# Kernel tuning notes

Hardware: AMD Instinct MI355X
Metric: run time of the kernel (lower is better)

Reference implementation:

```python
import jax, jax.numpy as jnp
import numpy as np

N_NODES = 100000
N_EDGES = 3200000
NUM_GRAPHS = 512


def _glorot(key, shape):
    fan_in, fan_out = shape[0], shape[1]
    lim = float(np.sqrt(6.0 / (fan_in + fan_out)))
    return jax.random.uniform(key, shape, jnp.float32, -lim, lim)


def setup_inputs() -> dict:
    key = jax.random.key(0)
    ks = jax.random.split(key, 12)
    x = jax.random.normal(ks[0], (N_NODES, 3), jnp.float32)
    edge_index = jax.random.randint(ks[1], (2, N_EDGES), 0, N_NODES, jnp.int64)
    batch = jnp.sort(jax.random.randint(ks[2], (N_NODES,), 0, NUM_GRAPHS, jnp.int64))
    return {
        'x': x,
        'edge_index': edge_index,
        'batch': batch,
        'W1': _glorot(ks[3], (3, 32)), 'b1': jnp.zeros((32,), jnp.float32),
        'W2': _glorot(ks[4], (32, 64)), 'b2': jnp.zeros((64,), jnp.float32),
        'W3': _glorot(ks[5], (64, 64)), 'b3': jnp.zeros((64,), jnp.float32),
        'lW1': _glorot(ks[6], (64, 32)), 'lb1': jnp.zeros((32,), jnp.float32),
        'lW2': _glorot(ks[7], (32, 5)), 'lb2': jnp.zeros((5,), jnp.float32),
    }


def gcn_conv(x, src, dst, W, b, n):
    # PyG GCNConv: add self-loops, symmetric deg^{-1/2} normalization,
    # linear transform then gather-scale-scatter aggregation.
    loop = jnp.arange(n, dtype=src.dtype)
    s = jnp.concatenate([src, loop])
    d = jnp.concatenate([dst, loop])
    deg = jax.ops.segment_sum(jnp.ones_like(d, dtype=x.dtype), d, num_segments=n)
    dinv = jnp.where(deg > 0, jax.lax.rsqrt(deg), 0.0)
    norm = dinv[s] * dinv[d]  # [E+N]
    h = x @ W                 # [N, out]
    out = jax.ops.segment_sum(h[s] * norm[:, None], d, num_segments=n)
    return out + b


def reference(x, edge_index, batch, W1, b1, W2, b2, W3, b3, lW1, lb1, lW2, lb2):
    src, dst = edge_index[0], edge_index[1]
    n = x.shape[0]
    h = jax.nn.relu(gcn_conv(x, src, dst, W1, b1, n))
    h = jax.nn.relu(gcn_conv(h, src, dst, W2, b2, n))
    h = gcn_conv(h, src, dst, W3, b3, n)
    pooled = jax.ops.segment_sum(h, batch, num_segments=NUM_GRAPHS)  # [G, 64]
    z = jax.nn.relu(pooled @ lW1 + lb1)
    z = z @ lW2 + lb2
    # original applies log_softmax over dim=0 (the graph axis)
    return jax.nn.log_softmax(z, axis=0)
```

## Files before the change

kernel.cpp:

```cpp
#include <hip/hip_runtime.h>
#include <hip/hip_fp16.h>

#define N_GRAPHS 512
#define NB 1563
#define KNODE 64
#define CAP 3072
#define EPW 8192
#define NWMAX 400


__global__ void k_part2(const int4* __restrict__ src4, const int4* __restrict__ dst4,
                        unsigned* __restrict__ ebuf2, unsigned* __restrict__ P, int E, int nw) {
    __shared__ int dstc[EPW];
    __shared__ unsigned hist[NB];
    __shared__ unsigned tsum[256];
    int w = blockIdx.x, t = threadIdx.x;
    int e0 = w * EPW;
    int cnt = E - e0 < EPW ? E - e0 : EPW;
    int cnt4 = cnt >> 2;
    for (int i = t; i < NB; i += 256) hist[i] = 0;
    __syncthreads();
    const int4* d4 = dst4 + (e0 >> 2);
    const int4* s4 = src4 + (e0 >> 2);
    for (int i = t; i < cnt4; i += 256) {
        int4 d = d4[i];
        dstc[4 * i + 0] = d.x; dstc[4 * i + 1] = d.y;
        dstc[4 * i + 2] = d.z; dstc[4 * i + 3] = d.w;
        atomicAdd(&hist[d.x >> 6], 1u);
        atomicAdd(&hist[d.y >> 6], 1u);
        atomicAdd(&hist[d.z >> 6], 1u);
        atomicAdd(&hist[d.w >> 6], 1u);
    }
    __syncthreads();
    const int PT7 = 7;
    unsigned loc[PT7];
    int base = t * PT7;
    unsigned s = 0;
#pragma unroll
    for (int k = 0; k < PT7; ++k) {
        int idx = base + k;
        unsigned v = (idx < NB) ? hist[idx] : 0u;
        loc[k] = s;
        s += v;
    }
    tsum[t] = s;
    __syncthreads();
    for (int off = 1; off < 256; off <<= 1) {
        unsigned u = (t >= off) ? tsum[t - off] : 0u;
        __syncthreads();
        tsum[t] += u;
        __syncthreads();
    }
    unsigned toff = tsum[t] - s;
#pragma unroll
    for (int k = 0; k < PT7; ++k) {
        int idx = base + k;
        if (idx < NB) {
            unsigned cb = ((k < PT7 - 1) ? loc[k + 1] : s) - loc[k];
            unsigned st = toff + loc[k];
            P[(size_t)w * NB + idx] = (st << 16) | cb;
        }
    }
    __syncthreads();
#pragma unroll
    for (int k = 0; k < PT7; ++k) {
        int idx = base + k;
        if (idx < NB) hist[idx] = toff + loc[k];
    }
    __syncthreads();
    for (int i = t; i < cnt4; i += 256) {
        int4 sv = s4[i];
#pragma unroll
        for (int q = 0; q < 4; ++q) {
            int d = dstc[4 * i + q];
            int svv = q == 0 ? sv.x : q == 1 ? sv.y : q == 2 ? sv.z : sv.w;
            int bkt = d >> 6;
            unsigned pos = atomicAdd(&hist[bkt], 1u);
            ebuf2[(size_t)e0 + pos] = (unsigned)svv | ((unsigned)(d & 63) << 20);
        }
    }
}


__global__ void kT(const unsigned* __restrict__ P, unsigned* __restrict__ PT, int nw) {
    __shared__ unsigned tile[32][33];
    int bw = blockIdx.x;
    int bb = blockIdx.y;
    int tx = threadIdx.x & 31, ty = threadIdx.x >> 5;
#pragma unroll
    for (int r = 0; r < 32; r += 8) {
        int w = bw * 32 + ty + r;
        int b = bb * 32 + tx;
        tile[ty + r][tx] = (w < nw && b < NB) ? P[(size_t)w * NB + b] : 0u;
    }
    __syncthreads();
#pragma unroll
    for (int r = 0; r < 32; r += 8) {
        int b = bb * 32 + ty + r;
        int w = bw * 32 + tx;
        if (b < NB && w < nw) PT[(size_t)b * nw + w] = tile[tx][ty + r];
    }
}


__global__ void k_csr2(const unsigned* __restrict__ ebuf2, const unsigned* __restrict__ PT,
                       unsigned* __restrict__ ebufF, int* __restrict__ gCnt,
                       int2* __restrict__ rows, float* __restrict__ dinv, int n, int nw) {
    __shared__ unsigned ec[CAP];
    __shared__ unsigned info[NWMAX];
    __shared__ unsigned coff[NWMAX];
    __shared__ unsigned tsum[256];
    __shared__ int bins[KNODE], pfx[KNODE];
    int b = blockIdx.x, t = threadIdx.x;
    for (int w = t; w < nw; w += 256) info[w] = PT[(size_t)b * nw + w];
    __syncthreads();
    unsigned l0, l1, s = 0;
    {
        int i0 = t * 2, i1 = t * 2 + 1;
        unsigned v0 = (i0 < nw) ? (info[i0] & 0xFFFFu) : 0u;
        unsigned v1 = (i1 < nw) ? (info[i1] & 0xFFFFu) : 0u;
        l0 = 0; l1 = v0; s = v0 + v1;
    }
    tsum[t] = s;
    __syncthreads();
    for (int off = 1; off < 256; off <<= 1) {
        unsigned u = (t >= off) ? tsum[t - off] : 0u;
        __syncthreads();
        tsum[t] += u;
        __syncthreads();
    }
    unsigned toff = tsum[t] - s;
    {
        int i0 = t * 2, i1 = t * 2 + 1;
        if (i0 < nw) coff[i0] = toff + l0;
        if (i1 < nw) coff[i1] = toff + l1;
    }
    __syncthreads();
    int total = (int)tsum[255];
    int cnt = total < CAP ? total : CAP;
    if (t == 0) gCnt[b] = cnt;
    for (int w = t; w < nw; w += 256) {
        unsigned inf = info[w];
        unsigned st = inf >> 16, c = inf & 0xFFFFu;
        unsigned d0 = coff[w];
        const unsigned* src = ebuf2 + (size_t)w * EPW + st;
        for (unsigned k = 0; k < c; ++k) {
            unsigned p = d0 + k;
            if (p < (unsigned)CAP) ec[p] = src[k];
        }
    }
    if (t < KNODE) bins[t] = 0;
    __syncthreads();
    for (int i = t; i < cnt; i += 256) atomicAdd(&bins[ec[i] >> 20], 1);
    __syncthreads();
    if (t == 0) {
        int a = 0;
        for (int i = 0; i < KNODE; ++i) { pfx[i] = a; a += bins[i]; }
    }
    __syncthreads();
    if (t < KNODE) {
        int node = b * KNODE + t;
        if (node < n) {
            rows[node] = make_int2(b * CAP + pfx[t], bins[t]);
            dinv[node] = rsqrtf((float)(bins[t] + 1));
        }
    }
    if (t < KNODE) bins[t] = pfx[t];
    __syncthreads();
    for (int i = t; i < cnt; i += 256) {
        unsigned p = ec[i];
        int pp = atomicAdd(&bins[p >> 20], 1);
        ebufF[(size_t)b * CAP + pp] = p & 0xFFFFFu;
    }
}


__global__ void k_pre1(const float* __restrict__ x, const float* __restrict__ dinv,
                       float4* __restrict__ ts0, int n) {
    int i = blockIdx.x * 256 + threadIdx.x;
    if (i >= n) return;
    float d = dinv[i];
    ts0[i] = make_float4(d * x[3 * i], d * x[3 * i + 1], d * x[3 * i + 2], 0.f);
}


__global__ void k_agg1(const float4* __restrict__ ts0, const unsigned* __restrict__ esrc,
                       const int2* __restrict__ rows, const float* __restrict__ dinv,
                       float4* __restrict__ o1, int n) {
    int node = blockIdx.x * 256 + threadIdx.x;
    if (node >= n) return;
    int2 rc = rows[node];
    int s0 = rc.x, deg = rc.y;
    float4 a = ts0[node];
    int e = 0;
    for (; e + 4 <= deg; e += 4) {
        unsigned i0 = esrc[s0 + e + 0];
        unsigned i1 = esrc[s0 + e + 1];
        unsigned i2 = esrc[s0 + e + 2];
        unsigned i3 = esrc[s0 + e + 3];
        float4 v0 = ts0[i0], v1 = ts0[i1], v2 = ts0[i2], v3 = ts0[i3];
        a.x += v0.x + v1.x + v2.x + v3.x;
        a.y += v0.y + v1.y + v2.y + v3.y;
        a.z += v0.z + v1.z + v2.z + v3.z;
    }
    for (; e < deg; ++e) {
        float4 v = ts0[esrc[s0 + e]];
        a.x += v.x; a.y += v.y; a.z += v.z;
    }
    float d = dinv[node];
    o1[node] = make_float4(d * a.x, d * a.y, d * a.z, 0.f);
}


__global__ void k_t1(const float4* __restrict__ o1, const float* __restrict__ W1,
                     const float* __restrict__ b1, const float* __restrict__ dinv,
                     uint4* __restrict__ ts1, int n) {
    __shared__ float sW[96];
    __shared__ float sb[32];
    int t = threadIdx.x;
    if (t < 96) sW[t] = W1[t];
    if (t < 32) sb[t] = b1[t];
    __syncthreads();
    int ln = t >> 2, c = t & 3;
    int node = blockIdx.x * 64 + ln;
    if (node >= n) return;
    float4 o = o1[node];
    float d = dinv[node];
    float r[8];
#pragma unroll
    for (int k = 0; k < 8; ++k) {
        int j = c * 8 + k;
        float h = o.x * sW[j] + o.y * sW[32 + j] + o.z * sW[64 + j] + sb[j];
        r[k] = fmaxf(h, 0.f) * d;
    }
    __half2 h0 = __floats2half2_rn(r[0], r[1]);
    __half2 h1 = __floats2half2_rn(r[2], r[3]);
    __half2 h2 = __floats2half2_rn(r[4], r[5]);
    __half2 h3 = __floats2half2_rn(r[6], r[7]);
    uint4 w;
    w.x = *(unsigned*)&h0; w.y = *(unsigned*)&h1;
    w.z = *(unsigned*)&h2; w.w = *(unsigned*)&h3;
    ts1[(size_t)node * 4 + c] = w;
}


template <int NSLICE>
__global__ void k_aggW(const uint4* __restrict__ ts, const unsigned* __restrict__ ebuf,
                       const int* __restrict__ gCnt, const int2* __restrict__ rows,
                       const float* __restrict__ dinv, uint4* __restrict__ out, int n) {
    __shared__ unsigned eidx[CAP];
    __shared__ int cursor;
    int i = blockIdx.x;
    int b, slice;
    if (NSLICE == 1) {
        b = i; slice = 0;
    } else {
        int xcd = i & 7;
        slice = xcd & 1;
        b = (i >> 3) * 4 + (xcd >> 1);
    }
    if (b >= NB) return;
    int t = threadIdx.x;
    int cnt = gCnt[b];
    if (cnt > CAP) cnt = CAP;
    int bBase = b * CAP;
    const uint4* ebuf4 = (const uint4*)(ebuf + bBase);
    int cnt4 = (cnt + 3) >> 2;
    for (int k = t; k < cnt4; k += 128) ((uint4*)eidx)[k] = ebuf4[k];
    if (t == 0) cursor = 0;
    __syncthreads();

    const uint4* tss = ts + (size_t)slice * n * 4;
    int lane = t & 3;
    for (;;) {
        int my;
        if (lane == 0) my = atomicAdd(&cursor, 1);
        my = __shfl(my, 0, 4);
        if (my >= KNODE) break;
        int node = b * KNODE + my;
        if (node >= n) continue;
        int2 rc = rows[node];
        int ls = rc.x - bBase;
        int deg = rc.y;
        float2 a0, a1, a2, a3;
        {
            uint4 sv = tss[(size_t)node * 4 + lane];
            a0 = __half22float2(*(__half2*)&sv.x);
            a1 = __half22float2(*(__half2*)&sv.y);
            a2 = __half22float2(*(__half2*)&sv.z);
            a3 = __half22float2(*(__half2*)&sv.w);
        }
        int e = 0;
        for (; e + 4 <= deg; e += 4) {
            unsigned s0 = eidx[ls + e + 0];
            unsigned s1 = eidx[ls + e + 1];
            unsigned s2 = eidx[ls + e + 2];
            unsigned s3 = eidx[ls + e + 3];
            uint4 v0 = tss[(size_t)s0 * 4 + lane];
            uint4 v1 = tss[(size_t)s1 * 4 + lane];
            uint4 v2 = tss[(size_t)s2 * 4 + lane];
            uint4 v3 = tss[(size_t)s3 * 4 + lane];
            float2 f;
            f = __half22float2(*(__half2*)&v0.x); a0.x += f.x; a0.y += f.y;
            f = __half22float2(*(__half2*)&v0.y); a1.x += f.x; a1.y += f.y;
            f = __half22float2(*(__half2*)&v0.z); a2.x += f.x; a2.y += f.y;
            f = __half22float2(*(__half2*)&v0.w); a3.x += f.x; a3.y += f.y;
            f = __half22float2(*(__half2*)&v1.x); a0.x += f.x; a0.y += f.y;
            f = __half22float2(*(__half2*)&v1.y); a1.x += f.x; a1.y += f.y;
            f = __half22float2(*(__half2*)&v1.z); a2.x += f.x; a2.y += f.y;
            f = __half22float2(*(__half2*)&v1.w); a3.x += f.x; a3.y += f.y;
            f = __half22float2(*(__half2*)&v2.x); a0.x += f.x; a0.y += f.y;
            f = __half22float2(*(__half2*)&v2.y); a1.x += f.x; a1.y += f.y;
            f = __half22float2(*(__half2*)&v2.z); a2.x += f.x; a2.y += f.y;
            f = __half22float2(*(__half2*)&v2.w); a3.x += f.x; a3.y += f.y;
            f = __half22float2(*(__half2*)&v3.x); a0.x += f.x; a0.y += f.y;
            f = __half22float2(*(__half2*)&v3.y); a1.x += f.x; a1.y += f.y;
            f = __half22float2(*(__half2*)&v3.z); a2.x += f.x; a2.y += f.y;
            f = __half22float2(*(__half2*)&v3.w); a3.x += f.x; a3.y += f.y;
        }
        for (; e < deg; ++e) {
            unsigned s = eidx[ls + e];
            uint4 v = tss[(size_t)s * 4 + lane];
            float2 f;
            f = __half22float2(*(__half2*)&v.x); a0.x += f.x; a0.y += f.y;
            f = __half22float2(*(__half2*)&v.y); a1.x += f.x; a1.y += f.y;
            f = __half22float2(*(__half2*)&v.z); a2.x += f.x; a2.y += f.y;
            f = __half22float2(*(__half2*)&v.w); a3.x += f.x; a3.y += f.y;
        }
        float dd = dinv[node];
        __half2 o0 = __floats2half2_rn(dd * a0.x, dd * a0.y);
        __half2 o1 = __floats2half2_rn(dd * a1.x, dd * a1.y);
        __half2 o2 = __floats2half2_rn(dd * a2.x, dd * a2.y);
        __half2 o3 = __floats2half2_rn(dd * a3.x, dd * a3.y);
        uint4 w;
        w.x = *(unsigned*)&o0; w.y = *(unsigned*)&o1;
        w.z = *(unsigned*)&o2; w.w = *(unsigned*)&o3;
        out[(size_t)node * (NSLICE * 4) + slice * 4 + lane] = w;
    }
}


__global__ void k_t2(const uint4* __restrict__ o2, const float* __restrict__ W2,
                     const float* __restrict__ b2, const float* __restrict__ dinv,
                     uint4* __restrict__ ts2, int n) {
    __shared__ uint4 sO[128];
    __shared__ float sW[32 * 64];
    __shared__ float sb[64];
    int t = threadIdx.x;
    for (int i = t; i < 32 * 64; i += 256) sW[i] = W2[i];
    if (t < 64) sb[t] = b2[t];
    int node0 = blockIdx.x * 32;
    if (t < 128) {
        int nd = node0 + (t >> 2);
        sO[t] = (nd < n) ? o2[(size_t)node0 * 4 + t] : make_uint4(0, 0, 0, 0);
    }
    __syncthreads();
    int ln = t >> 3, c = t & 7;
    int node = node0 + ln;
    if (node >= n) return;
    const __half2* sOh = (const __half2*)sO;
    float acc[8];
#pragma unroll
    for (int k = 0; k < 8; ++k) acc[k] = sb[c * 8 + k];
#pragma unroll
    for (int i2 = 0; i2 < 16; ++i2) {
        float2 av = __half22float2(sOh[ln * 16 + i2]);
        const float* w0 = &sW[(2 * i2) * 64 + c * 8];
        const float* w1 = &sW[(2 * i2 + 1) * 64 + c * 8];
#pragma unroll
        for (int k = 0; k < 8; ++k) acc[k] += av.x * w0[k] + av.y * w1[k];
    }
    float d = dinv[node];
    float r[8];
#pragma unroll
    for (int k = 0; k < 8; ++k) r[k] = fmaxf(acc[k], 0.f) * d;
    __half2 h0 = __floats2half2_rn(r[0], r[1]);
    __half2 h1 = __floats2half2_rn(r[2], r[3]);
    __half2 h2 = __floats2half2_rn(r[4], r[5]);
    __half2 h3 = __floats2half2_rn(r[6], r[7]);
    uint4 w;
    w.x = *(unsigned*)&h0; w.y = *(unsigned*)&h1;
    w.z = *(unsigned*)&h2; w.w = *(unsigned*)&h3;
    ts2[((size_t)(c >> 2) * n + node) * 4 + (c & 3)] = w;
}


__global__ void k_pool(const __half2* __restrict__ h, const int* __restrict__ batch,
                       float* __restrict__ pooled, float* __restrict__ cntf, int n) {
    const int NBK = 32;
    int lane = threadIdx.x & 31;
    int sub = threadIdx.x >> 5;
    int n0 = (blockIdx.x * 8 + sub) * NBK;
    if (n0 >= n) return;
    int nend = n0 + NBK < n ? n0 + NBK : n;
    float2 acc = make_float2(0.f, 0.f);
    float rc = 0.f;
    int gcur = batch[n0];
    for (int i = n0; i < nend; ++i) {
        int g = batch[i];
        if (g != gcur) {
            atomicAdd(&pooled[gcur * 64 + 2 * lane], acc.x);
            atomicAdd(&pooled[gcur * 64 + 2 * lane + 1], acc.y);
            if (lane == 0) atomicAdd(&cntf[gcur], rc);
            acc = make_float2(0.f, 0.f);
            rc = 0.f;
            gcur = g;
        }
        float2 v = __half22float2(h[(size_t)i * 32 + lane]);
        acc.x += v.x;
        acc.y += v.y;
        rc += 1.f;
    }
    atomicAdd(&pooled[gcur * 64 + 2 * lane], acc.x);
    atomicAdd(&pooled[gcur * 64 + 2 * lane + 1], acc.y);
    if (lane == 0) atomicAdd(&cntf[gcur], rc);
}


#define GPB 4
__global__ void k_z(const float* __restrict__ P, const float* __restrict__ cntf,
                    const float* __restrict__ W3, const float* __restrict__ b3,
                    const float* __restrict__ lW1, const float* __restrict__ lb1,
                    const float* __restrict__ lW2, const float* __restrict__ lb2,
                    float* __restrict__ z) {
    __shared__ float sW3[64 * 64];
    __shared__ float sW1[64 * 32];
    __shared__ float sW2[32 * 5];
    __shared__ float sb3[64], sb1[32], sb2[5];
    __shared__ float sP[GPB][64];
    __shared__ float sH[GPB][64];
    __shared__ float sT[GPB][32];
    int t = threadIdx.x;
    for (int i = t; i < 64 * 64; i += 256) sW3[i] = W3[i];
    for (int i = t; i < 64 * 32; i += 256) sW1[i] = lW1[i];
    for (int i = t; i < 32 * 5; i += 256) sW2[i] = lW2[i];
    if (t < 64) sb3[t] = b3[t];
    if (t < 32) sb1[t] = lb1[t];
    if (t < 5) sb2[t] = lb2[t];
    int g0 = blockIdx.x * GPB;
    for (int i = t; i < GPB * 64; i += 256) sP[i >> 6][i & 63] = P[(size_t)g0 * 64 + i];
    __syncthreads();
    int lg = t >> 6;
    int j = t & 63;
    int g = g0 + lg;
    float cg = cntf[g];
    float a = cg * sb3[j];
#pragma unroll 8
    for (int i = 0; i < 64; ++i) a += sP[lg][i] * sW3[i * 64 + j];
    sH[lg][j] = a;
    __syncthreads();
    if (j < 32) {
        float a2 = sb1[j];
#pragma unroll 8
        for (int i = 0; i < 64; ++i) a2 += sH[lg][i] * sW1[i * 32 + j];
        sT[lg][j] = fmaxf(a2, 0.f);
    }
    __syncthreads();
    if (j < 5) {
        float a3 = sb2[j];
#pragma unroll
        for (int i = 0; i < 32; ++i) a3 += sT[lg][i] * sW2[i * 5 + j];
        z[g * 5 + j] = a3;
    }
}


__global__ void k_lsm(const float* __restrict__ z, float* __restrict__ out) {
    __shared__ float red[512];
    int g = threadIdx.x;
#pragma unroll
    for (int c = 0; c < 5; ++c) {
        float v = z[g * 5 + c];
        red[g] = v;
        __syncthreads();
        for (int off = 256; off > 0; off >>= 1) {
            if (g < off) red[g] = fmaxf(red[g], red[g + off]);
            __syncthreads();
        }
        float m = red[0];
        __syncthreads();
        red[g] = expf(v - m);
        __syncthreads();
        for (int off = 256; off > 0; off >>= 1) {
            if (g < off) red[g] += red[g + off];
            __syncthreads();
        }
        float lse = m + logf(red[0]);
        __syncthreads();
        out[g * 5 + c] = v - lse;
    }
}


extern "C" void kernel_launch(void* const* d_in, const int* in_sizes, int n_in,
                              void* d_out, int out_size, void* d_ws, size_t ws_size,
                              hipStream_t stream) {
    const float* x   = (const float*)d_in[0];
    const int* ei    = (const int*)d_in[1];
    const int* batch = (const int*)d_in[2];
    const float* W1  = (const float*)d_in[3];
    const float* b1  = (const float*)d_in[4];
    const float* W2  = (const float*)d_in[5];
    const float* b2  = (const float*)d_in[6];
    const float* W3  = (const float*)d_in[7];
    const float* b3  = (const float*)d_in[8];
    const float* lW1 = (const float*)d_in[9];
    const float* lb1 = (const float*)d_in[10];
    const float* lW2 = (const float*)d_in[11];
    const float* lb2 = (const float*)d_in[12];

    const int N = in_sizes[0] / 3;
    const int E = in_sizes[1] / 2;
    const int* src = ei;
    const int* dst = ei + E;
    const int nw = (E + EPW - 1) / EPW;

    char* ws = (char*)d_ws;
    size_t off = 0;
    auto alloc = [&](size_t bytes) -> void* {
        void* p = ws + off;
        off = (off + bytes + 255) & ~(size_t)255;
        return p;
    };

    int*      gCnt    = (int*)alloc((size_t)NB * 4);
    float*    dinv    = (float*)alloc((size_t)N * 4);
    int2*     rows    = (int2*)alloc((size_t)N * 8);
    unsigned* ebuf2   = (unsigned*)alloc((size_t)nw * EPW * 4);
    unsigned* P       = (unsigned*)alloc((size_t)nw * NB * 4);
    unsigned* PT      = (unsigned*)alloc((size_t)NB * nw * 4);
    unsigned* ebufF   = (unsigned*)alloc((size_t)NB * CAP * 4);
    uint4*    ts1     = (uint4*)alloc((size_t)N * 4 * 16);
    uint4*    o2      = (uint4*)alloc((size_t)N * 4 * 16);
    uint4*    ts2     = (uint4*)alloc((size_t)N * 8 * 16);
    float*    pooledP = (float*)alloc((size_t)N_GRAPHS * 64 * 4);
    float*    cntf    = (float*)alloc((size_t)N_GRAPHS * 4);
    float*    zbuf    = (float*)alloc((size_t)N_GRAPHS * 5 * 4);
    float4*   ts0     = (float4*)P;
    float4*   o1      = (float4*)PT;
    uint4*    o3      = (uint4*)ebuf2;

    hipMemsetAsync(pooledP, 0, (size_t)N_GRAPHS * 64 * 4, stream);
    hipMemsetAsync(cntf, 0, (size_t)N_GRAPHS * 4, stream);

    k_part2<<<nw, 256, 0, stream>>>((const int4*)src, (const int4*)dst, ebuf2, P, E, nw);
    dim3 gT((nw + 31) / 32, (NB + 31) / 32);
    kT<<<gT, 256, 0, stream>>>(P, PT, nw);
    k_csr2<<<NB, 256, 0, stream>>>(ebuf2, PT, ebufF, gCnt, rows, dinv, N, nw);

    k_pre1<<<(N + 255) / 256, 256, 0, stream>>>(x, dinv, ts0, N);
    k_agg1<<<(N + 255) / 256, 256, 0, stream>>>(ts0, ebufF, rows, dinv, o1, N);
    k_t1<<<(N + 63) / 64, 256, 0, stream>>>(o1, W1, b1, dinv, ts1, N);

    k_aggW<1><<<NB, 128, 0, stream>>>(ts1, ebufF, gCnt, rows, dinv, o2, N);
    k_t2<<<(N + 31) / 32, 256, 0, stream>>>(o2, W2, b2, dinv, ts2, N);

    k_aggW<2><<<8 * ((NB + 3) / 4), 128, 0, stream>>>(ts2, ebufF, gCnt, rows, dinv, o3, N);

    k_pool<<<(N + 8 * 32 - 1) / (8 * 32), 256, 0, stream>>>((const __half2*)o3, batch,
                                                            pooledP, cntf, N);
    k_z<<<N_GRAPHS / GPB, 256, 0, stream>>>(pooledP, cntf, W3, b3, lW1, lb1, lW2, lb2, zbuf);
    k_lsm<<<1, 512, 0, stream>>>(zbuf, (float*)d_out);
}
```

Measured before the change: 252.2 us.

## Split feature tables into narrower per-XCD slices for layer 2 and 3 aggregation

```diff
diff --git a/kernel.cpp b/kernel.cpp
--- a/kernel.cpp
+++ b/kernel.cpp
@@ -240,42 +240,38 @@
     uint4 w;
     w.x = *(unsigned*)&h0; w.y = *(unsigned*)&h1;
     w.z = *(unsigned*)&h2; w.w = *(unsigned*)&h3;
-    ts1[(size_t)node * 4 + c] = w;
+    ts1[((size_t)(c >> 1) * n + node) * 2 + (c & 1)] = w;
 }
 
 
 template <int NSLICE>
-__global__ void k_aggW(const uint4* __restrict__ ts, const unsigned* __restrict__ ebuf,
+__global__ void k_aggP(const uint4* __restrict__ ts, const unsigned* __restrict__ ebuf,
                        const int* __restrict__ gCnt, const int2* __restrict__ rows,
                        const float* __restrict__ dinv, uint4* __restrict__ out, int n) {
+    const int XPG = 8 / NSLICE;
     __shared__ unsigned eidx[CAP];
     __shared__ int cursor;
     int i = blockIdx.x;
-    int b, slice;
-    if (NSLICE == 1) {
-        b = i; slice = 0;
-    } else {
-        int xcd = i & 7;
-        slice = xcd & 1;
-        b = (i >> 3) * 4 + (xcd >> 1);
-    }
+    int xcd = i & 7;
+    int slice = xcd % NSLICE;
+    int b = (i >> 3) * XPG + xcd / NSLICE;
     if (b >= NB) return;
     int t = threadIdx.x;
     int cnt = gCnt[b];
     if (cnt > CAP) cnt = CAP;
     int bBase = b * CAP;
-    const uint4* ebuf4 = (const uint4*)(ebuf + bBase);
+    const uint4* e4 = (const uint4*)(ebuf + bBase);
     int cnt4 = (cnt + 3) >> 2;
-    for (int k = t; k < cnt4; k += 128) ((uint4*)eidx)[k] = ebuf4[k];
+    for (int k = t; k < cnt4; k += 128) ((uint4*)eidx)[k] = e4[k];
     if (t == 0) cursor = 0;
     __syncthreads();
 
-    const uint4* tss = ts + (size_t)slice * n * 4;
-    int lane = t & 3;
+    const uint4* tss = ts + (size_t)slice * n * 2;
+    int lane = t & 1;
     for (;;) {
         int my;
         if (lane == 0) my = atomicAdd(&cursor, 1);
-        my = __shfl(my, 0, 4);
+        my = __shfl(my, 0, 2);
         if (my >= KNODE) break;
         int node = b * KNODE + my;
         if (node >= n) continue;
@@ -284,22 +280,22 @@
         int deg = rc.y;
         float2 a0, a1, a2, a3;
         {
-            uint4 sv = tss[(size_t)node * 4 + lane];
+            uint4 sv = tss[(size_t)node * 2 + lane];
             a0 = __half22float2(*(__half2*)&sv.x);
             a1 = __half22float2(*(__half2*)&sv.y);
             a2 = __half22float2(*(__half2*)&sv.z);
             a3 = __half22float2(*(__half2*)&sv.w);
         }
         int e = 0;
-        for (; e + 4 <= deg; e += 4) {
-            unsigned s0 = eidx[ls + e + 0];
-            unsigned s1 = eidx[ls + e + 1];
-            unsigned s2 = eidx[ls + e + 2];
-            unsigned s3 = eidx[ls + e + 3];
-            uint4 v0 = tss[(size_t)s0 * 4 + lane];
-            uint4 v1 = tss[(size_t)s1 * 4 + lane];
-            uint4 v2 = tss[(size_t)s2 * 4 + lane];
-            uint4 v3 = tss[(size_t)s3 * 4 + lane];
+        for (; e + 8 <= deg; e += 8) {
+            uint4 v0 = tss[(size_t)eidx[ls + e + 0] * 2 + lane];
+            uint4 v1 = tss[(size_t)eidx[ls + e + 1] * 2 + lane];
+            uint4 v2 = tss[(size_t)eidx[ls + e + 2] * 2 + lane];
+            uint4 v3 = tss[(size_t)eidx[ls + e + 3] * 2 + lane];
+            uint4 v4 = tss[(size_t)eidx[ls + e + 4] * 2 + lane];
+            uint4 v5 = tss[(size_t)eidx[ls + e + 5] * 2 + lane];
+            uint4 v6 = tss[(size_t)eidx[ls + e + 6] * 2 + lane];
+            uint4 v7 = tss[(size_t)eidx[ls + e + 7] * 2 + lane];
             float2 f;
             f = __half22float2(*(__half2*)&v0.x); a0.x += f.x; a0.y += f.y;
             f = __half22float2(*(__half2*)&v0.y); a1.x += f.x; a1.y += f.y;
@@ -317,10 +313,25 @@
             f = __half22float2(*(__half2*)&v3.y); a1.x += f.x; a1.y += f.y;
             f = __half22float2(*(__half2*)&v3.z); a2.x += f.x; a2.y += f.y;
             f = __half22float2(*(__half2*)&v3.w); a3.x += f.x; a3.y += f.y;
+            f = __half22float2(*(__half2*)&v4.x); a0.x += f.x; a0.y += f.y;
+            f = __half22float2(*(__half2*)&v4.y); a1.x += f.x; a1.y += f.y;
+            f = __half22float2(*(__half2*)&v4.z); a2.x += f.x; a2.y += f.y;
+            f = __half22float2(*(__half2*)&v4.w); a3.x += f.x; a3.y += f.y;
+            f = __half22float2(*(__half2*)&v5.x); a0.x += f.x; a0.y += f.y;
+            f = __half22float2(*(__half2*)&v5.y); a1.x += f.x; a1.y += f.y;
+            f = __half22float2(*(__half2*)&v5.z); a2.x += f.x; a2.y += f.y;
+            f = __half22float2(*(__half2*)&v5.w); a3.x += f.x; a3.y += f.y;
+            f = __half22float2(*(__half2*)&v6.x); a0.x += f.x; a0.y += f.y;
+            f = __half22float2(*(__half2*)&v6.y); a1.x += f.x; a1.y += f.y;
+            f = __half22float2(*(__half2*)&v6.z); a2.x += f.x; a2.y += f.y;
+            f = __half22float2(*(__half2*)&v6.w); a3.x += f.x; a3.y += f.y;
+            f = __half22float2(*(__half2*)&v7.x); a0.x += f.x; a0.y += f.y;
+            f = __half22float2(*(__half2*)&v7.y); a1.x += f.x; a1.y += f.y;
+            f = __half22float2(*(__half2*)&v7.z); a2.x += f.x; a2.y += f.y;
+            f = __half22float2(*(__half2*)&v7.w); a3.x += f.x; a3.y += f.y;
         }
         for (; e < deg; ++e) {
-            unsigned s = eidx[ls + e];
-            uint4 v = tss[(size_t)s * 4 + lane];
+            uint4 v = tss[(size_t)eidx[ls + e] * 2 + lane];
             float2 f;
             f = __half22float2(*(__half2*)&v.x); a0.x += f.x; a0.y += f.y;
             f = __half22float2(*(__half2*)&v.y); a1.x += f.x; a1.y += f.y;
@@ -335,7 +346,7 @@
         uint4 w;
         w.x = *(unsigned*)&o0; w.y = *(unsigned*)&o1;
         w.z = *(unsigned*)&o2; w.w = *(unsigned*)&o3;
-        out[(size_t)node * (NSLICE * 4) + slice * 4 + lane] = w;
+        out[(size_t)node * (NSLICE * 2) + slice * 2 + lane] = w;
     }
 }
 
@@ -381,7 +392,7 @@
     uint4 w;
     w.x = *(unsigned*)&h0; w.y = *(unsigned*)&h1;
     w.z = *(unsigned*)&h2; w.w = *(unsigned*)&h3;
-    ts2[((size_t)(c >> 2) * n + node) * 4 + (c & 3)] = w;
+    ts2[((size_t)(c >> 1) * n + node) * 2 + (c & 1)] = w;
 }
 
 
@@ -552,10 +563,10 @@
     k_agg1<<<(N + 255) / 256, 256, 0, stream>>>(ts0, ebufF, rows, dinv, o1, N);
     k_t1<<<(N + 63) / 64, 256, 0, stream>>>(o1, W1, b1, dinv, ts1, N);
 
-    k_aggW<1><<<NB, 128, 0, stream>>>(ts1, ebufF, gCnt, rows, dinv, o2, N);
+    k_aggP<2><<<8 * ((NB + 3) / 4), 128, 0, stream>>>(ts1, ebufF, gCnt, rows, dinv, o2, N);
     k_t2<<<(N + 31) / 32, 256, 0, stream>>>(o2, W2, b2, dinv, ts2, N);
 
-    k_aggW<2><<<8 * ((NB + 3) / 4), 128, 0, stream>>>(ts2, ebufF, gCnt, rows, dinv, o3, N);
+    k_aggP<4><<<8 * ((NB + 1) / 2), 128, 0, stream>>>(ts2, ebufF, gCnt, rows, dinv, o3, N);
 
     k_pool<<<(N + 8 * 32 - 1) / (8 * 32), 256, 0, stream>>>((const __half2*)o3, batch,
                                                             pooledP, cntf, N);
```

After: 264.8 us. 5.0% more time.

## Split aggregation blocks per half-bucket and use interleaved 64-wide feature layout

Applied to the files above, without the earlier changes.

```diff
diff --git a/kernel.cpp b/kernel.cpp
--- a/kernel.cpp
+++ b/kernel.cpp
@@ -7,6 +7,7 @@
 #define CAP 3072
 #define EPW 8192
 #define NWMAX 400
+#define HCAP 2048
 
 
 __global__ void k_part2(const int4* __restrict__ src4, const int4* __restrict__ dst4,
@@ -244,47 +245,47 @@
 }
 
 
-template <int NSLICE>
-__global__ void k_aggW(const uint4* __restrict__ ts, const unsigned* __restrict__ ebuf,
+template <int LPN>
+__global__ void k_aggN(const uint4* __restrict__ ts, const unsigned* __restrict__ ebuf,
                        const int* __restrict__ gCnt, const int2* __restrict__ rows,
                        const float* __restrict__ dinv, uint4* __restrict__ out, int n) {
-    __shared__ unsigned eidx[CAP];
+    __shared__ unsigned eidx[HCAP];
     __shared__ int cursor;
-    int i = blockIdx.x;
-    int b, slice;
-    if (NSLICE == 1) {
-        b = i; slice = 0;
-    } else {
-        int xcd = i & 7;
-        slice = xcd & 1;
-        b = (i >> 3) * 4 + (xcd >> 1);
-    }
-    if (b >= NB) return;
+    int blk = blockIdx.x;
+    int b = blk >> 1, half = blk & 1;
+    int n0 = b * KNODE + half * 32;
+    if (n0 >= n) return;
     int t = threadIdx.x;
-    int cnt = gCnt[b];
-    if (cnt > CAP) cnt = CAP;
     int bBase = b * CAP;
-    const uint4* ebuf4 = (const uint4*)(ebuf + bBase);
-    int cnt4 = (cnt + 3) >> 2;
-    for (int k = t; k < cnt4; k += 128) ((uint4*)eidx)[k] = ebuf4[k];
+    int cntb = gCnt[b];
+    if (cntb > CAP) cntb = CAP;
+    int startL = rows[n0].x - bBase;
+    int endL;
+    int nmid = b * KNODE + 32;
+    if (half == 0 && nmid < n) endL = rows[nmid].x - bBase;
+    else endL = cntb;
+    int myCnt = endL - startL;
+    if (myCnt > HCAP) myCnt = HCAP;
+    const unsigned* esrc = ebuf + bBase + startL;
+    for (int k = t; k < myCnt; k += 128) eidx[k] = esrc[k];
     if (t == 0) cursor = 0;
     __syncthreads();
 
-    const uint4* tss = ts + (size_t)slice * n * 4;
-    int lane = t & 3;
+    int lane = t & (LPN - 1);
     for (;;) {
         int my;
         if (lane == 0) my = atomicAdd(&cursor, 1);
-        my = __shfl(my, 0, 4);
-        if (my >= KNODE) break;
-        int node = b * KNODE + my;
+        my = __shfl(my, (t / LPN) * LPN, 64);
+        if (my >= 32) break;
+        int node = n0 + my;
         if (node >= n) continue;
         int2 rc = rows[node];
-        int ls = rc.x - bBase;
+        int ls = rc.x - bBase - startL;
         int deg = rc.y;
+        if (ls + deg > myCnt) deg = myCnt - ls > 0 ? myCnt - ls : 0;
         float2 a0, a1, a2, a3;
         {
-            uint4 sv = tss[(size_t)node * 4 + lane];
+            uint4 sv = ts[(size_t)node * LPN + lane];
             a0 = __half22float2(*(__half2*)&sv.x);
             a1 = __half22float2(*(__half2*)&sv.y);
             a2 = __half22float2(*(__half2*)&sv.z);
@@ -292,14 +293,10 @@
         }
         int e = 0;
         for (; e + 4 <= deg; e += 4) {
-            unsigned s0 = eidx[ls + e + 0];
-            unsigned s1 = eidx[ls + e + 1];
-            unsigned s2 = eidx[ls + e + 2];
-            unsigned s3 = eidx[ls + e + 3];
-            uint4 v0 = tss[(size_t)s0 * 4 + lane];
-            uint4 v1 = tss[(size_t)s1 * 4 + lane];
-            uint4 v2 = tss[(size_t)s2 * 4 + lane];
-            uint4 v3 = tss[(size_t)s3 * 4 + lane];
+            uint4 v0 = ts[(size_t)eidx[ls + e + 0] * LPN + lane];
+            uint4 v1 = ts[(size_t)eidx[ls + e + 1] * LPN + lane];
+            uint4 v2 = ts[(size_t)eidx[ls + e + 2] * LPN + lane];
+            uint4 v3 = ts[(size_t)eidx[ls + e + 3] * LPN + lane];
             float2 f;
             f = __half22float2(*(__half2*)&v0.x); a0.x += f.x; a0.y += f.y;
             f = __half22float2(*(__half2*)&v0.y); a1.x += f.x; a1.y += f.y;
@@ -319,8 +316,7 @@
             f = __half22float2(*(__half2*)&v3.w); a3.x += f.x; a3.y += f.y;
         }
         for (; e < deg; ++e) {
-            unsigned s = eidx[ls + e];
-            uint4 v = tss[(size_t)s * 4 + lane];
+            uint4 v = ts[(size_t)eidx[ls + e] * LPN + lane];
             float2 f;
             f = __half22float2(*(__half2*)&v.x); a0.x += f.x; a0.y += f.y;
             f = __half22float2(*(__half2*)&v.y); a1.x += f.x; a1.y += f.y;
@@ -335,7 +331,7 @@
         uint4 w;
         w.x = *(unsigned*)&o0; w.y = *(unsigned*)&o1;
         w.z = *(unsigned*)&o2; w.w = *(unsigned*)&o3;
-        out[(size_t)node * (NSLICE * 4) + slice * 4 + lane] = w;
+        out[(size_t)node * LPN + lane] = w;
     }
 }
 
@@ -381,7 +377,7 @@
     uint4 w;
     w.x = *(unsigned*)&h0; w.y = *(unsigned*)&h1;
     w.z = *(unsigned*)&h2; w.w = *(unsigned*)&h3;
-    ts2[((size_t)(c >> 2) * n + node) * 4 + (c & 3)] = w;
+    ts2[(size_t)node * 8 + c] = w;
 }
 
 
@@ -552,10 +548,10 @@
     k_agg1<<<(N + 255) / 256, 256, 0, stream>>>(ts0, ebufF, rows, dinv, o1, N);
     k_t1<<<(N + 63) / 64, 256, 0, stream>>>(o1, W1, b1, dinv, ts1, N);
 
-    k_aggW<1><<<NB, 128, 0, stream>>>(ts1, ebufF, gCnt, rows, dinv, o2, N);
+    k_aggN<4><<<NB * 2, 128, 0, stream>>>(ts1, ebufF, gCnt, rows, dinv, o2, N);
     k_t2<<<(N + 31) / 32, 256, 0, stream>>>(o2, W2, b2, dinv, ts2, N);
 
-    k_aggW<2><<<8 * ((NB + 3) / 4), 128, 0, stream>>>(ts2, ebufF, gCnt, rows, dinv, o3, N);
+    k_aggN<8><<<NB * 2, 128, 0, stream>>>(ts2, ebufF, gCnt, rows, dinv, o3, N);
 
     k_pool<<<(N + 8 * 32 - 1) / (8 * 32), 256, 0, stream>>>((const __half2*)o3, batch,
                                                             pooledP, cntf, N);
```

Measured after the change: 240.5 us. -4.6%, faster.
